# Optimization experiments

Hardware: AMD Instinct MI355X
Metric: run time of the kernel (lower is better)

The kernel has to match this reference:

```python
import jax, jax.numpy as jnp
import numpy as np

B, S, D, H = 4, 2048, 1024, 16
DH = D // H  # head dim = 64


def setup_inputs() -> dict:
    key = jax.random.key(0)
    ks = jax.random.split(key, 7)
    q = jax.random.normal(ks[0], (B, S, D), dtype=jnp.float32)
    k = jax.random.normal(ks[1], (B, S, D), dtype=jnp.float32)
    v = jax.random.normal(ks[2], (B, S, D), dtype=jnp.float32)
    mask = jax.random.uniform(ks[3], (1, S, S), dtype=jnp.float32)
    sc = 1.0 / np.sqrt(D)
    Wq = jax.random.normal(ks[4], (D, D), dtype=jnp.float32) * sc
    Wk = jax.random.normal(ks[5], (D, D), dtype=jnp.float32) * sc
    Wv = jax.random.normal(ks[6], (D, D), dtype=jnp.float32) * sc
    return {"q": q, "k": k, "v": v, "mask": mask, "Wq": Wq, "Wk": Wk, "Wv": Wv}


def reference(q, k, v, mask, Wq, Wk, Wv):
    # Linear projections (no bias), then split hidden into H heads.
    # tf.concat(tf.split(x, H, axis=2), axis=0) == reshape to (B,S,H,DH);
    # the final split/concat restores channel order [head0, head1, ...],
    # i.e. a plain (B,S,H,DH)->(B,S,D) reshape.
    qh = (q @ Wq).reshape(B, S, H, DH)
    kh = (k @ Wk).reshape(B, S, H, DH)
    vh = (v @ Wv).reshape(B, S, H, DH)
    score = jnp.einsum("bqhd,bkhd->bhqk", qh, kh) / jnp.sqrt(
        jnp.asarray(DH, dtype=q.dtype))
    # multiplicative mask applied BEFORE softmax (broadcast (1,Sq,Sk))
    score = score * mask[:, None, :, :][0:1].squeeze(0) if False else score * mask  # mask (1,Sq,Sk) broadcasts over (B,H,Sq,Sk)
    attn = jax.nn.softmax(score, axis=-1)
    out = jnp.einsum("bhqk,bkhd->bqhd", attn, vh).reshape(B, S, D)
    return out
```

## Files before the change

kernel.cpp:

```cpp
#include <hip/hip_runtime.h>

#define B_  4
#define S_  2048
#define D_  1024
#define H_  16
#define DH_ 64

typedef __attribute__((ext_vector_type(8))) short bf16x8;
typedef __attribute__((ext_vector_type(4))) float f32x4;
typedef __attribute__((ext_vector_type(16))) float f32x16;
typedef __attribute__((ext_vector_type(4))) unsigned short u16x4;

__device__ __forceinline__ unsigned short f2bf(float f) {
  union { float f; unsigned int u; } x; x.f = f;
  unsigned int u = x.u;
  unsigned int r = (u + 0x7fffu + ((u >> 16) & 1u)) >> 16;
  return (unsigned short)r;
}

__device__ __forceinline__ int cvtpk(float lo, float hi) {
  unsigned r;
  asm("v_cvt_pk_bf16_f32 %0, %1, %2" : "=v"(r) : "v"(lo), "v"(hi));
  return (int)r;
}

__global__ __launch_bounds__(256) void wtrans_kernel(const float* __restrict__ W0,
                                                     const float* __restrict__ W1,
                                                     const float* __restrict__ W2,
                                                     unsigned short* __restrict__ Wt) {
  __shared__ float t[32][33];
  const int z = blockIdx.z;
  const float* W = (z == 0) ? W0 : ((z == 1) ? W1 : W2);
  unsigned short* O = Wt + (size_t)z * (D_ * D_);
  const int n0 = blockIdx.x * 32, k0 = blockIdx.y * 32;
  const int tx = threadIdx.x, ty = threadIdx.y;
#pragma unroll
  for (int i = 0; i < 4; i++) t[ty + i * 8][tx] = W[(size_t)(k0 + ty + i * 8) * D_ + n0 + tx];
  __syncthreads();
#pragma unroll
  for (int i = 0; i < 4; i++)
    O[(size_t)(n0 + ty + i * 8) * D_ + k0 + tx] = f2bf(t[tx][ty + i * 8]);
}

__global__ __launch_bounds__(256) void proj_kernel(const float* __restrict__ X0,
                                                   const float* __restrict__ X1,
                                                   const float* __restrict__ X2,
                                                   const unsigned short* __restrict__ Wt,
                                                   unsigned short* __restrict__ Y0) {
  __shared__ unsigned short Alds[128 * 72];
  __shared__ unsigned short Blds[128 * 72];
  const int z = blockIdx.z;
  const float* X = (z == 0) ? X0 : ((z == 1) ? X1 : X2);
  const unsigned short* Wz = Wt + (size_t)z * (D_ * D_);
  unsigned short* Y = Y0 + (size_t)z * ((size_t)B_ * S_ * D_);
  const float osc = (z == 0) ? 0.18033688f : 1.0f;

  const int tid = threadIdx.x;
  const int lane = tid & 63, w = tid >> 6;
  const int wr = w >> 1, wc = w & 1;
  const int l15 = lane & 15, lg = lane >> 4;
  const int r0 = blockIdx.y * 128, c0 = blockIdx.x * 128;

  f32x4 acc[4][4];
#pragma unroll
  for (int m = 0; m < 4; m++)
#pragma unroll
    for (int n = 0; n < 4; n++) acc[m][n] = (f32x4){0.f, 0.f, 0.f, 0.f};

  for (int kt = 0; kt < 16; ++kt) {
    __syncthreads();
    {
      const int rr = tid >> 4, cf = (tid & 15) * 4;
#pragma unroll
      for (int p = 0; p < 8; p++) {
        int row = rr + p * 16;
        float4 xv = *(const float4*)(X + (size_t)(r0 + row) * D_ + kt * 64 + cf);
        u16x4 bb = { f2bf(xv.x), f2bf(xv.y), f2bf(xv.z), f2bf(xv.w) };
        *(u16x4*)(&Alds[row * 72 + cf]) = bb;
      }
      const int rb = tid >> 3, cb = tid & 7;
#pragma unroll
      for (int p = 0; p < 4; p++) {
        int row = rb + p * 32;
        bf16x8 wv = *(const bf16x8*)(Wz + (size_t)(c0 + row) * D_ + kt * 64 + cb * 8);
        *(bf16x8*)(&Blds[row * 72 + cb * 8]) = wv;
      }
    }
    __syncthreads();

    bf16x8 af[4][2];
#pragma unroll
    for (int m = 0; m < 4; m++)
#pragma unroll
      for (int kc = 0; kc < 2; kc++)
        af[m][kc] = *(const bf16x8*)(&Alds[(wr * 64 + m * 16 + l15) * 72 + kc * 32 + lg * 8]);
#pragma unroll
    for (int n = 0; n < 4; n++) {
      bf16x8 bfr[2];
#pragma unroll
      for (int kc = 0; kc < 2; kc++)
        bfr[kc] = *(const bf16x8*)(&Blds[(wc * 64 + n * 16 + l15) * 72 + kc * 32 + lg * 8]);
#pragma unroll
      for (int m = 0; m < 4; m++)
#pragma unroll
        for (int kc = 0; kc < 2; kc++)
          acc[m][n] = __builtin_amdgcn_mfma_f32_16x16x32_bf16(af[m][kc], bfr[kc], acc[m][n], 0, 0, 0);
    }
  }

#pragma unroll
  for (int m = 0; m < 4; m++)
#pragma unroll
    for (int n = 0; n < 4; n++)
#pragma unroll
      for (int r = 0; r < 4; r++) {
        int row = r0 + wr * 64 + m * 16 + lg * 4 + r;
        int col = c0 + wc * 64 + n * 16 + l15;
        Y[(size_t)row * D_ + col] = f2bf(acc[m][n][r] * osc);
      }
}

__global__ __launch_bounds__(256) void attn_kernel(
    const unsigned short* __restrict__ qh,
    const unsigned short* __restrict__ kh,
    const unsigned short* __restrict__ vh,
    const float* __restrict__ mask,
    float* __restrict__ out) {
  __shared__ __align__(16) unsigned short K_lds[2][64 * 72];
  __shared__ __align__(16) unsigned short V_lds[2][64 * 72];

  const int tid = threadIdx.x;
  const int lane = tid & 63, w = tid >> 6;
  const int l31 = lane & 31, hf = lane >> 5;
  const int q0 = blockIdx.x * 128;
  const int h = blockIdx.y, b = blockIdx.z;
  const size_t head = (size_t)b * S_ * D_ + h * DH_;
  const int qrow = q0 + w * 32 + l31;

  bf16x8 bq[4];
  {
    const unsigned short* qp = qh + head + (size_t)qrow * D_;
#pragma unroll
    for (int ds = 0; ds < 4; ds++) bq[ds] = *(const bf16x8*)(qp + ds * 16 + hf * 8);
  }

  const int rr = tid >> 3, cc = tid & 7;
  const unsigned short* kbase = kh + head + (size_t)rr * D_ + cc * 8;
  const unsigned short* vbase = vh + head + (size_t)rr * D_ + cc * 8;

  f32x16 o_acc[2];
#pragma unroll
  for (int dt = 0; dt < 2; dt++)
#pragma unroll
    for (int r = 0; r < 16; r++) o_acc[dt][r] = 0.f;
  float m_r = -INFINITY, l_r = 0.f;

  bf16x8 kreg[2], vreg[2];
#pragma unroll
  for (int p = 0; p < 2; p++) {
    kreg[p] = *(const bf16x8*)(kbase + (size_t)p * 32 * D_);
    vreg[p] = *(const bf16x8*)(vbase + (size_t)p * 32 * D_);
  }
#pragma unroll
  for (int p = 0; p < 2; p++) {
    int row = rr + p * 32;
    *(bf16x8*)(&K_lds[0][row * 72 + cc * 8]) = kreg[p];
#pragma unroll
    for (int j = 0; j < 8; j++) {
      int d = cc * 8 + j;
      int byt = (d * 72 + row) * 2;
      byt ^= ((d >> 3) & 7) << 4;
      *(unsigned short*)((char*)&V_lds[0][0] + byt) = (unsigned short)vreg[p][j];
    }
  }

  for (int kt = 0; kt < 32; kt++) {
    const int cur = kt & 1;

    bf16x8 kreg2[2], vreg2[2];
    if (kt + 1 < 32) {
      const size_t tb = (size_t)(kt + 1) * 64 * D_;
#pragma unroll
      for (int p = 0; p < 2; p++) {
        kreg2[p] = *(const bf16x8*)(kbase + tb + (size_t)p * 32 * D_);
        vreg2[p] = *(const bf16x8*)(vbase + tb + (size_t)p * 32 * D_);
      }
    }

    __syncthreads();

    f32x16 sacc[2];
#pragma unroll
    for (int ct = 0; ct < 2; ct++)
#pragma unroll
      for (int r = 0; r < 16; r++) sacc[ct][r] = 0.f;
#pragma unroll
    for (int ds = 0; ds < 4; ds++)
#pragma unroll
      for (int ct = 0; ct < 2; ct++) {
        bf16x8 ak = *(const bf16x8*)(&K_lds[cur][(ct * 32 + l31) * 72 + ds * 16 + hf * 8]);
        sacc[ct] = __builtin_amdgcn_mfma_f32_32x32x16_bf16(ak, bq[ds], sacc[ct], 0, 0, 0);
      }

    const float* mrow = mask + (size_t)qrow * S_ + kt * 64 + hf * 4;
#pragma unroll
    for (int ct = 0; ct < 2; ct++)
#pragma unroll
      for (int rq = 0; rq < 4; rq++) {
        float4 mk = *(const float4*)(mrow + ct * 32 + rq * 8);
        sacc[ct][rq * 4 + 0] *= mk.x;
        sacc[ct][rq * 4 + 1] *= mk.y;
        sacc[ct][rq * 4 + 2] *= mk.z;
        sacc[ct][rq * 4 + 3] *= mk.w;
      }

    float tm = sacc[0][0];
#pragma unroll
    for (int r = 1; r < 16; r++) tm = fmaxf(tm, sacc[0][r]);
#pragma unroll
    for (int r = 0; r < 16; r++) tm = fmaxf(tm, sacc[1][r]);
    tm = fmaxf(tm, __shfl_xor(tm, 32));

    float mn;
    if (__any(tm > m_r + 8.0f)) {
      mn = fmaxf(m_r, tm);
      float alpha = exp2f(m_r - mn);
      m_r = mn;
      l_r *= alpha;
#pragma unroll
      for (int dt = 0; dt < 2; dt++)
#pragma unroll
        for (int r = 0; r < 16; r++) o_acc[dt][r] *= alpha;
    } else {
      mn = m_r;
    }

    float rs = 0.f;
#pragma unroll
    for (int ct = 0; ct < 2; ct++)
#pragma unroll
      for (int r = 0; r < 16; r++) {
        float p = exp2f(sacc[ct][r] - mn);
        sacc[ct][r] = p;
        rs += p;
      }
    rs += __shfl_xor(rs, 32);
    l_r += rs;

    bf16x8 bfp[4];
#pragma unroll
    for (int s = 0; s < 4; s++) {
      const int ct = s >> 1, rb = (s & 1) * 8;
      int L1 = cvtpk(sacc[ct][rb + 0], sacc[ct][rb + 1]);
      int L2 = cvtpk(sacc[ct][rb + 2], sacc[ct][rb + 3]);
      int H1 = cvtpk(sacc[ct][rb + 4], sacc[ct][rb + 5]);
      int H2 = cvtpk(sacc[ct][rb + 6], sacc[ct][rb + 7]);
      int xL1 = __shfl_xor(L1, 32), xL2 = __shfl_xor(L2, 32);
      int xH1 = __shfl_xor(H1, 32), xH2 = __shfl_xor(H2, 32);
      union { int u[4]; bf16x8 v; } cv;
      cv.u[0] = hf ? xH1 : L1;
      cv.u[1] = hf ? xH2 : L2;
      cv.u[2] = hf ? H1 : xL1;
      cv.u[3] = hf ? H2 : xL2;
      bfp[s] = cv.v;
    }

#pragma unroll
    for (int dt = 0; dt < 2; dt++) {
      const int d0 = dt * 32 + l31;
      const int bbase = d0 * 144;
      const int swz = ((d0 >> 3) & 7) << 4;
#pragma unroll
      for (int s = 0; s < 4; s++) {
        int byt = (bbase + (s * 16 + hf * 8) * 2) ^ swz;
        bf16x8 av = *(const bf16x8*)((const char*)&V_lds[cur][0] + byt);
        o_acc[dt] = __builtin_amdgcn_mfma_f32_32x32x16_bf16(av, bfp[s], o_acc[dt], 0, 0, 0);
      }
    }

    if (kt + 1 < 32) {
#pragma unroll
      for (int p = 0; p < 2; p++) {
        int row = rr + p * 32;
        *(bf16x8*)(&K_lds[cur ^ 1][row * 72 + cc * 8]) = kreg2[p];
#pragma unroll
        for (int j = 0; j < 8; j++) {
          int d = cc * 8 + j;
          int byt = (d * 72 + row) * 2;
          byt ^= ((d >> 3) & 7) << 4;
          *(unsigned short*)((char*)&V_lds[cur ^ 1][0] + byt) = (unsigned short)vreg2[p][j];
        }
      }
    }
  }

  const float invl = 1.0f / l_r;
  float* op = out + (size_t)(b * S_ + qrow) * D_ + h * DH_;
#pragma unroll
  for (int dt = 0; dt < 2; dt++)
#pragma unroll
    for (int rq = 0; rq < 4; rq++) {
      float4 ov = { o_acc[dt][rq * 4 + 0] * invl, o_acc[dt][rq * 4 + 1] * invl,
                    o_acc[dt][rq * 4 + 2] * invl, o_acc[dt][rq * 4 + 3] * invl };
      *(float4*)(op + dt * 32 + rq * 8 + hf * 4) = ov;
    }
}

extern "C" void kernel_launch(void* const* d_in, const int* in_sizes, int n_in,
                              void* d_out, int out_size, void* d_ws, size_t ws_size,
                              hipStream_t stream) {
  const float* q = (const float*)d_in[0];
  const float* k = (const float*)d_in[1];
  const float* v = (const float*)d_in[2];
  const float* mask = (const float*)d_in[3];
  const float* Wq = (const float*)d_in[4];
  const float* Wk = (const float*)d_in[5];
  const float* Wv = (const float*)d_in[6];

  char* ws = (char*)d_ws;
  const size_t SZ_PROJ = (size_t)B_ * S_ * D_ * 2;
  unsigned short* qh = (unsigned short*)(ws);
  unsigned short* kh = (unsigned short*)(ws + SZ_PROJ);
  unsigned short* vh = (unsigned short*)(ws + 2 * SZ_PROJ);
  unsigned short* Wt = (unsigned short*)(ws + 3 * SZ_PROJ);

  wtrans_kernel<<<dim3(D_ / 32, D_ / 32, 3), dim3(32, 8), 0, stream>>>(Wq, Wk, Wv, Wt);
  proj_kernel<<<dim3(D_ / 128, (B_ * S_) / 128, 3), 256, 0, stream>>>(q, k, v, Wt, qh);
  attn_kernel<<<dim3(S_ / 128, H_, B_), 256, 0, stream>>>(qh, kh, vh, mask, (float*)d_out);
}
```

Baseline: 343.1 us.

## Double attention query tile per block to 512 threads and streamline K/V pipeline sync

The attention block now covers 256 query rows with 8 waves instead of 128 rows with 4 waves. Each thread now loads a single K/V row chunk per tile, so K/V global traffic and LDS staging are shared by twice as many queries. The loop drops the top-of-iteration __syncthreads and uses one explicit waitcnt plus barrier after filling the next buffer. It also raises wave priority around the MFMA blocks and switches the row max and row sum to tree reductions. The cost is fewer, larger blocks, which lowers grid parallelism and raises per-block register and occupancy pressure.

```diff
diff --git a/kernel.cpp b/kernel.cpp
--- a/kernel.cpp
+++ b/kernel.cpp
@@ -120,7 +120,7 @@
       }
 }
 
-__global__ __launch_bounds__(256) void attn_kernel(
+__global__ __launch_bounds__(512) void attn_kernel(
     const unsigned short* __restrict__ qh,
     const unsigned short* __restrict__ kh,
     const unsigned short* __restrict__ vh,
@@ -132,7 +132,7 @@
   const int tid = threadIdx.x;
   const int lane = tid & 63, w = tid >> 6;
   const int l31 = lane & 31, hf = lane >> 5;
-  const int q0 = blockIdx.x * 128;
+  const int q0 = blockIdx.x * 256;
   const int h = blockIdx.y, b = blockIdx.z;
   const size_t head = (size_t)b * S_ * D_ + h * DH_;
   const int qrow = q0 + w * 32 + l31;
@@ -155,45 +155,38 @@
     for (int r = 0; r < 16; r++) o_acc[dt][r] = 0.f;
   float m_r = -INFINITY, l_r = 0.f;
 
-  bf16x8 kreg[2], vreg[2];
-#pragma unroll
-  for (int p = 0; p < 2; p++) {
-    kreg[p] = *(const bf16x8*)(kbase + (size_t)p * 32 * D_);
-    vreg[p] = *(const bf16x8*)(vbase + (size_t)p * 32 * D_);
-  }
-#pragma unroll
-  for (int p = 0; p < 2; p++) {
-    int row = rr + p * 32;
-    *(bf16x8*)(&K_lds[0][row * 72 + cc * 8]) = kreg[p];
+  {
+    bf16x8 kreg = *(const bf16x8*)(kbase);
+    bf16x8 vreg = *(const bf16x8*)(vbase);
+    *(bf16x8*)(&K_lds[0][rr * 72 + cc * 8]) = kreg;
 #pragma unroll
     for (int j = 0; j < 8; j++) {
       int d = cc * 8 + j;
-      int byt = (d * 72 + row) * 2;
+      int byt = (d * 72 + rr) * 2;
       byt ^= ((d >> 3) & 7) << 4;
-      *(unsigned short*)((char*)&V_lds[0][0] + byt) = (unsigned short)vreg[p][j];
-    }
+      *(unsigned short*)((char*)&V_lds[0][0] + byt) = (unsigned short)vreg[j];
+    }
+    asm volatile("s_waitcnt lgkmcnt(0)" ::: "memory");
+    __builtin_amdgcn_s_barrier();
   }
 
   for (int kt = 0; kt < 32; kt++) {
     const int cur = kt & 1;
-
-    bf16x8 kreg2[2], vreg2[2];
-    if (kt + 1 < 32) {
+    const bool more = (kt + 1 < 32);
+
+    bf16x8 kreg2, vreg2;
+    if (more) {
       const size_t tb = (size_t)(kt + 1) * 64 * D_;
-#pragma unroll
-      for (int p = 0; p < 2; p++) {
-        kreg2[p] = *(const bf16x8*)(kbase + tb + (size_t)p * 32 * D_);
-        vreg2[p] = *(const bf16x8*)(vbase + tb + (size_t)p * 32 * D_);
-      }
-    }
-
-    __syncthreads();
+      kreg2 = *(const bf16x8*)(kbase + tb);
+      vreg2 = *(const bf16x8*)(vbase + tb);
+    }
 
     f32x16 sacc[2];
 #pragma unroll
     for (int ct = 0; ct < 2; ct++)
 #pragma unroll
       for (int r = 0; r < 16; r++) sacc[ct][r] = 0.f;
+    __builtin_amdgcn_s_setprio(1);
 #pragma unroll
     for (int ds = 0; ds < 4; ds++)
 #pragma unroll
@@ -201,6 +194,7 @@
         bf16x8 ak = *(const bf16x8*)(&K_lds[cur][(ct * 32 + l31) * 72 + ds * 16 + hf * 8]);
         sacc[ct] = __builtin_amdgcn_mfma_f32_32x32x16_bf16(ak, bq[ds], sacc[ct], 0, 0, 0);
       }
+    __builtin_amdgcn_s_setprio(0);
 
     const float* mrow = mask + (size_t)qrow * S_ + kt * 64 + hf * 4;
 #pragma unroll
@@ -214,12 +208,14 @@
         sacc[ct][rq * 4 + 3] *= mk.w;
       }
 
-    float tm = sacc[0][0];
-#pragma unroll
-    for (int r = 1; r < 16; r++) tm = fmaxf(tm, sacc[0][r]);
-#pragma unroll
-    for (int r = 0; r < 16; r++) tm = fmaxf(tm, sacc[1][r]);
-    tm = fmaxf(tm, __shfl_xor(tm, 32));
+    float red[16];
+#pragma unroll
+    for (int i = 0; i < 16; i++) red[i] = fmaxf(sacc[0][i], sacc[1][i]);
+#pragma unroll
+    for (int off = 8; off >= 1; off >>= 1)
+#pragma unroll
+      for (int i = 0; i < off; i++) red[i] = fmaxf(red[i], red[i + off]);
+    float tm = fmaxf(red[0], __shfl_xor(red[0], 32));
 
     float mn;
     if (__any(tm > m_r + 8.0f)) {
@@ -235,17 +231,19 @@
       mn = m_r;
     }
 
-    float rs = 0.f;
 #pragma unroll
     for (int ct = 0; ct < 2; ct++)
 #pragma unroll
-      for (int r = 0; r < 16; r++) {
-        float p = exp2f(sacc[ct][r] - mn);
-        sacc[ct][r] = p;
-        rs += p;
-      }
-    rs += __shfl_xor(rs, 32);
-    l_r += rs;
+      for (int r = 0; r < 16; r++) sacc[ct][r] = exp2f(sacc[ct][r] - mn);
+
+    float sr[16];
+#pragma unroll
+    for (int i = 0; i < 16; i++) sr[i] = sacc[0][i] + sacc[1][i];
+#pragma unroll
+    for (int off = 8; off >= 1; off >>= 1)
+#pragma unroll
+      for (int i = 0; i < off; i++) sr[i] += sr[i + off];
+    l_r += sr[0] + __shfl_xor(sr[0], 32);
 
     bf16x8 bfp[4];
 #pragma unroll
@@ -265,6 +263,7 @@
       bfp[s] = cv.v;
     }
 
+    __builtin_amdgcn_s_setprio(1);
 #pragma unroll
     for (int dt = 0; dt < 2; dt++) {
       const int d0 = dt * 32 + l31;
@@ -277,20 +276,19 @@
         o_acc[dt] = __builtin_amdgcn_mfma_f32_32x32x16_bf16(av, bfp[s], o_acc[dt], 0, 0, 0);
       }
     }
-
-    if (kt + 1 < 32) {
-#pragma unroll
-      for (int p = 0; p < 2; p++) {
-        int row = rr + p * 32;
-        *(bf16x8*)(&K_lds[cur ^ 1][row * 72 + cc * 8]) = kreg2[p];
-#pragma unroll
-        for (int j = 0; j < 8; j++) {
-          int d = cc * 8 + j;
-          int byt = (d * 72 + row) * 2;
-          byt ^= ((d >> 3) & 7) << 4;
-          *(unsigned short*)((char*)&V_lds[cur ^ 1][0] + byt) = (unsigned short)vreg2[p][j];
-        }
-      }
+    __builtin_amdgcn_s_setprio(0);
+
+    if (more) {
+      *(bf16x8*)(&K_lds[cur ^ 1][rr * 72 + cc * 8]) = kreg2;
+#pragma unroll
+      for (int j = 0; j < 8; j++) {
+        int d = cc * 8 + j;
+        int byt = (d * 72 + rr) * 2;
+        byt ^= ((d >> 3) & 7) << 4;
+        *(unsigned short*)((char*)&V_lds[cur ^ 1][0] + byt) = (unsigned short)vreg2[j];
+      }
+      asm volatile("s_waitcnt lgkmcnt(0)" ::: "memory");
+      __builtin_amdgcn_s_barrier();
     }
   }
 
@@ -326,5 +324,5 @@
 
   wtrans_kernel<<<dim3(D_ / 32, D_ / 32, 3), dim3(32, 8), 0, stream>>>(Wq, Wk, Wv, Wt);
   proj_kernel<<<dim3(D_ / 128, (B_ * S_) / 128, 3), 256, 0, stream>>>(q, k, v, Wt, qh);
-  attn_kernel<<<dim3(S_ / 128, H_, B_), 256, 0, stream>>>(qh, kh, vh, mask, (float*)d_out);
-}
+  attn_kernel<<<dim3(S_ / 256, H_, B_), 512, 0, stream>>>(qh, kh, vh, mask, (float*)d_out);
+}
```

After: 389.1 us. +13.4%, slower.
